# Kernel optimization log

Measured on AMD Instinct MI355X. Metric: run time of the kernel, lower is better.

Reference implementation:

```python
import jax, jax.numpy as jnp
import numpy as np

N = 49152       # nodes
EH = 8192       # hyperedges (star nodes)
M = N + EH
F = 256         # num_features == expan_dim == MLP_hidden
D = 256
HEADS = 8
CHUNK = 1024
NE_N = 10 * N   # nnz of N x N sparse mats
NE_M = 10 * M   # nnz of M x M sparse mats


def spmm(row, col, val, X, n):
    # sparse [n, m] (COO) @ dense X [m, d] -> [n, d]
    return jax.ops.segment_sum(val[:, None] * X[col], row, num_segments=n)


def expan_net(x, row, col, val, Ws, bs, n):
    # 2-layer GCN: (A @ (X @ W) + b), ReLU between; dropout is identity in eval.
    h = spmm(row, col, val, x @ Ws[0], n) + bs[0]
    h = jax.nn.relu(h)
    return spmm(row, col, val, h @ Ws[1], n) + bs[1]


def chunked_mha(q, k, v, in_w, in_b, out_w, out_b):
    # torch nn.MultiheadAttention on unbatched [L, D] chunks of size CHUNK
    n, d = q.shape
    c = n // CHUNK
    dh = d // HEADS
    wq, wk, wv = jnp.split(in_w, 3, axis=0)
    bq, bk, bv = jnp.split(in_b, 3)
    def resh(t):
        return t.reshape(c, CHUNK, HEADS, dh)
    qh = resh(q @ wq.T + bq)
    kh = resh(k @ wk.T + bk)
    vh = resh(v @ wv.T + bv)
    scale = 1.0 / np.sqrt(dh)
    scores = jnp.einsum('clhe,cmhe->chlm', qh, kh) * scale  # [c,H,CHUNK,CHUNK]
    attn = jax.nn.softmax(scores, axis=-1)
    out = jnp.einsum('chlm,cmhe->clhe', attn, vh).reshape(n, d)
    return out @ out_w.T + out_b


def setup_inputs():
    key = jax.random.key(0)
    ks = iter(jax.random.split(key, 64))
    nrm = lambda shape, s=1.0: jax.random.normal(next(ks), shape, dtype=jnp.float32) * s
    uni = lambda shape: jax.random.uniform(next(ks), shape, dtype=jnp.float32)
    ridx = lambda shape, hi: jax.random.randint(next(ks), shape, 0, hi, dtype=jnp.int32)
    inp = {'x': nrm((N, F))}
    for nm, ne, hi in [('A_cg', NE_N, N), ('A_hyp', NE_N, N), ('A_sg', NE_M, M),
                       ('L_cg', NE_N, N), ('L_hyp', NE_N, N), ('L_sg', NE_M, M)]:
        inp[nm + '_row'] = ridx((ne,), hi)
        inp[nm + '_col'] = ridx((ne,), hi)
        inp[nm + '_val'] = uni((ne,)) * 0.1
    for p in ['cg', 'hg', 'sg']:
        inp[p + '_W'] = nrm((2, F, D), 0.05)
        inp[p + '_b'] = nrm((2, D), 0.05)
    for p in ['sn_hyp', 'sn_cg', 'sn_sg']:
        inp[p + '_W'] = nrm((D, D), 0.05)
        inp[p + '_b'] = nrm((D,), 0.05)
    for p in ['spa', 'spe']:
        for q in ['hyp', 'star', 'clq']:
            inp[f'{p}_{q}_W'] = nrm((D, D), 0.05)
            inp[f'{p}_{q}_b'] = nrm((D,), 0.05)
        inp[p + '_in_w'] = nrm((3 * D, D), 0.05)
        inp[p + '_in_b'] = nrm((3 * D,), 0.05)
        inp[p + '_out_w'] = nrm((D, D), 0.05)
        inp[p + '_out_b'] = nrm((D,), 0.05)
    return inp


def reference(x,
              A_cg_row, A_cg_col, A_cg_val, A_hyp_row, A_hyp_col, A_hyp_val,
              A_sg_row, A_sg_col, A_sg_val, L_cg_row, L_cg_col, L_cg_val,
              L_hyp_row, L_hyp_col, L_hyp_val, L_sg_row, L_sg_col, L_sg_val,
              cg_W, cg_b, hg_W, hg_b, sg_W, sg_b,
              sn_hyp_W, sn_hyp_b, sn_cg_W, sn_cg_b, sn_sg_W, sn_sg_b,
              spa_hyp_W, spa_hyp_b, spa_star_W, spa_star_b, spa_clq_W, spa_clq_b,
              spa_in_w, spa_in_b, spa_out_w, spa_out_b,
              spe_hyp_W, spe_hyp_b, spe_star_W, spe_star_b, spe_clq_W, spe_clq_b,
              spe_in_w, spe_in_b, spe_out_w, spe_out_b):
    n = x.shape[0]
    # star features: nodes first, zero-init hyperedge rows (v_mask == [True]*N+[False]*EH)
    x_star = jnp.concatenate([x, jnp.zeros((EH, x.shape[1]), x.dtype)], axis=0)
    # 1. Expansion graph convolutions
    cg_feat = expan_net(x, A_cg_row, A_cg_col, A_cg_val, cg_W, cg_b, n)
    hg_feat = expan_net(x, A_hyp_row, A_hyp_col, A_hyp_val, hg_W, hg_b, n)
    sg_feat = expan_net(x_star, A_sg_row, A_sg_col, A_sg_val, sg_W, sg_b, n + EH)
    X_star, S_star = sg_feat[:n], sg_feat[n:]
    # 2. SmoothNet: linear then Laplacian spmm
    X_hyp = spmm(L_hyp_row, L_hyp_col, L_hyp_val, hg_feat @ sn_hyp_W.T + sn_hyp_b, n)
    X_cg = spmm(L_cg_row, L_cg_col, L_cg_val, cg_feat @ sn_cg_W.T + sn_cg_b, n)
    X_sg = spmm(L_sg_row, L_sg_col, L_sg_val, sg_feat @ sn_sg_W.T + sn_sg_b, n + EH)
    # 3. TAA attention (chunked MHA, Q/K/V = hyp/star/clique projections)
    X_spectral = chunked_mha(X_hyp @ spe_hyp_W.T + spe_hyp_b,
                             X_cg @ spe_star_W.T + spe_star_b,
                             X_sg[:n] @ spe_clq_W.T + spe_clq_b,
                             spe_in_w, spe_in_b, spe_out_w, spe_out_b)
    X_spatial = chunked_mha(hg_feat @ spa_hyp_W.T + spa_hyp_b,
                            cg_feat @ spa_star_W.T + spa_star_b,
                            X_star @ spa_clq_W.T + spa_clq_b,
                            spa_in_w, spa_in_b, spa_out_w, spa_out_b)
    taa = jnp.concatenate([X_spatial, X_spectral], axis=1)
    return taa, X_star, S_star
```

## Files before the change

### kernel.cpp

```cpp
#include <hip/hip_runtime.h>

#define NN 49152
#define EHN 8192
#define MM (NN + EHN)
#define FD 256
#define DD 256
#define NHEADS 8
#define DHEAD 32
#define CHK 1024
#define NEN (10 * NN)
#define NEM (10 * MM)
#define ROWS_TOT (4 * NN + 2 * MM)
#define ETOT (4 * NEN + 2 * NEM)

typedef __bf16 bf16x8 __attribute__((ext_vector_type(8)));
typedef unsigned short u16x8 __attribute__((ext_vector_type(8)));
typedef float f32x4 __attribute__((ext_vector_type(4)));

static __device__ __forceinline__ unsigned short f2bf(float f) {
  unsigned int u = __float_as_uint(f);
  unsigned int r = (u + 0x7FFFu + ((u >> 16) & 1u)) >> 16;
  return (unsigned short)r;
}
static __device__ __forceinline__ float bf2f(unsigned short u) {
  return __uint_as_float((unsigned int)u << 16);
}
static __device__ __forceinline__ unsigned int cvtpk(float a, float b) {
  unsigned int r;
  asm("v_cvt_pk_bf16_f32 %0, %1, %2" : "=v"(r) : "v"(a), "v"(b));
  return r;
}

struct CastJobs {
  const float* src[8];
  unsigned short* dst[8];
  int trans[8];
};
__global__ __launch_bounds__(256) void cast_w8_kernel(CastJobs jobs)
{
  int job = blockIdx.x >> 8;
  int i = (blockIdx.x & 255) * 256 + threadIdx.x;
  int n = i >> 8, k = i & 255;
  const float* src = jobs.src[job];
  float f = jobs.trans[job] ? src[(size_t)k * 256 + n] : src[i];
  jobs.dst[job][i] = f2bf(f);
}

__global__ __launch_bounds__(256) void combine_w_kernel(
    const float* __restrict__ Bw, const float* __restrict__ Aw,
    const float* __restrict__ ab, const float* __restrict__ bb,
    unsigned short* __restrict__ Wc, float* __restrict__ bc, float fscale)
{
  int n = blockIdx.x, t = threadIdx.x;
  __shared__ float shB[256];
  __shared__ float red[256];
  shB[t] = Bw[n * 256 + t];
  __syncthreads();
  float acc = 0.0f;
  #pragma unroll 8
  for (int j = 0; j < 256; ++j) acc += shB[j] * Aw[j * 256 + t];
  Wc[n * 256 + t] = f2bf(acc * fscale);
  red[t] = shB[t] * ab[t];
  __syncthreads();
  for (int off = 128; off; off >>= 1) {
    if (t < off) red[t] += red[t + off];
    __syncthreads();
  }
  if (t == 0) bc[n] = (red[0] + bb[n]) * fscale;
}

__global__ __launch_bounds__(256) void mm256f_kernel(
    const float* __restrict__ A, const float* __restrict__ B,
    float* __restrict__ C)
{
  int n = blockIdx.x, t = threadIdx.x;
  __shared__ float sa[256];
  sa[t] = A[n * 256 + t];
  __syncthreads();
  float acc = 0.0f;
  #pragma unroll 8
  for (int j = 0; j < 256; ++j) acc += sa[j] * B[j * 256 + t];
  C[n * 256 + t] = acc;
}

__global__ __launch_bounds__(256) void mm256b_kernel(
    const float* __restrict__ A, const float* __restrict__ B,
    unsigned short* __restrict__ W, float fs)
{
  int n = blockIdx.x, t = threadIdx.x;
  __shared__ float sa[256];
  sa[t] = A[n * 256 + t];
  __syncthreads();
  float acc = 0.0f;
  #pragma unroll 8
  for (int j = 0; j < 256; ++j) acc += sa[j] * B[j * 256 + t];
  W[n * 256 + t] = f2bf(acc * fs);
}

__global__ __launch_bounds__(256) void mv256_kernel(
    const float* __restrict__ W, const float* __restrict__ v,
    const float* __restrict__ add, float* __restrict__ outv, float fs)
{
  int t = threadIdx.x;
  __shared__ float sv[256];
  sv[t] = v[t];
  __syncthreads();
  float acc = 0.0f;
  #pragma unroll 8
  for (int k = 0; k < 256; ++k) acc += W[t * 256 + k] * sv[k];
  if (add) acc += add[t];
  outv[t] = fs * acc;
}

template<int ABF, int OUTBF>
__global__ __launch_bounds__(256) void gemm2_kernel(
    const void* __restrict__ Ain, const unsigned short* __restrict__ Wt,
    const float* __restrict__ c0, const float* __restrict__ rs,
    const float* __restrict__ cvec, void* __restrict__ Cout,
    int ldc, int coff, int relu)
{
  __shared__ __align__(16) char sA[2][4096];
  __shared__ __align__(16) char sB[2][16384];
  const int tid = threadIdx.x, lane = tid & 63, wid = tid >> 6;
  const int l15 = lane & 15, l4 = lane >> 4;
  const int bm = blockIdx.x * 64;

  f32x4 acc[16] = {};
  const int ar = tid >> 2, akq = (tid & 3) * 8;
  const int bn = tid;

  float4 fa0, fa1;
  u16x8 ua;
  u16x8 rb0, rb1, rb2, rb3;
  auto stage_load = [&](int k0) {
    if (ABF) {
      ua = *(const u16x8*)((const unsigned short*)Ain +
                           (size_t)(bm + ar) * 256 + k0 + akq);
    } else {
      const float* ap = (const float*)Ain + (size_t)(bm + ar) * 256 + k0 + akq;
      fa0 = *(const float4*)ap;
      fa1 = *(const float4*)(ap + 4);
    }
    const unsigned short* bp = Wt + (size_t)bn * 256 + k0;
    rb0 = *(const u16x8*)bp;        rb1 = *(const u16x8*)(bp + 8);
    rb2 = *(const u16x8*)(bp + 16); rb3 = *(const u16x8*)(bp + 24);
  };
  auto stage_write = [&](int buf) {
    u16x8 va;
    if (ABF) {
      va = ua;
    } else {
      va[0] = f2bf(fa0.x); va[1] = f2bf(fa0.y); va[2] = f2bf(fa0.z); va[3] = f2bf(fa0.w);
      va[4] = f2bf(fa1.x); va[5] = f2bf(fa1.y); va[6] = f2bf(fa1.z); va[7] = f2bf(fa1.w);
    }
    int aa = ((ar << 6) + (akq << 1)) ^ ((ar & 7) << 4);
    *(u16x8*)(sA[buf] + aa) = va;
    int bb = (bn << 6) ^ ((bn & 7) << 4);
    *(u16x8*)(sB[buf] + bb) = rb0;
    *(u16x8*)(sB[buf] + (bb ^ 16)) = rb1;
    *(u16x8*)(sB[buf] + (bb ^ 32)) = rb2;
    *(u16x8*)(sB[buf] + (bb ^ 48)) = rb3;
  };

  stage_load(0);
  stage_write(0);
  __syncthreads();
  int cur = 0;
  for (int it = 0; it < 8; ++it) {
    if (it < 7) stage_load((it + 1) * 32);
    int ra = wid * 16 + l15;
    bf16x8 af = *(const bf16x8*)(sA[cur] + ((ra << 6) + (l4 << 4) ^ ((ra & 7) << 4)));
    #pragma unroll
    for (int n4 = 0; n4 < 16; ++n4) {
      int rn = n4 * 16 + l15;
      bf16x8 bf = *(const bf16x8*)(sB[cur] + ((rn << 6) + (l4 << 4) ^ ((rn & 7) << 4)));
      acc[n4] = __builtin_amdgcn_mfma_f32_16x16x32_bf16(af, bf, acc[n4], 0, 0, 0);
    }
    __syncthreads();
    if (it < 7) {
      stage_write(cur ^ 1);
      __syncthreads();
      cur ^= 1;
    }
  }
  const int row = bm + wid * 16 + l4 * 4;
  float rsv[4];
  if (rs) {
    #pragma unroll
    for (int j = 0; j < 4; ++j) rsv[j] = rs[row + j];
  }
  #pragma unroll
  for (int n4 = 0; n4 < 16; ++n4) {
    int col = n4 * 16 + l15;
    float base = c0 ? c0[col] : 0.0f;
    float cv = rs ? cvec[col] : 0.0f;
    #pragma unroll
    for (int j = 0; j < 4; ++j) {
      float v = acc[n4][j] + base;
      if (rs) v += rsv[j] * cv;
      if (relu) v = fmaxf(v, 0.0f);
      if (OUTBF)
        ((unsigned short*)Cout)[(size_t)(row + j) * 256 + col] = f2bf(v);
      else
        ((float*)Cout)[(size_t)(row + j) * ldc + coff + col] = v;
    }
  }
}

struct CooPtrs {
  const int* rw[6];
  const int* cl[6];
  const float* vl[6];
};
static __device__ __forceinline__ void coo_block_resolve(
    int b, int& g, int& eb, int& rb)
{
  if      (b < 1920) { g = 0; eb = 0;    rb = 0; }
  else if (b < 3840) { g = 1; eb = 1920; rb = NN; }
  else if (b < 6080) { g = 2; eb = 3840; rb = 2 * NN; }
  else if (b < 8000) { g = 3; eb = 6080; rb = 2 * NN + MM; }
  else if (b < 9920) { g = 4; eb = 8000; rb = 3 * NN + MM; }
  else               { g = 5; eb = 9920; rb = 4 * NN + MM; }
}

__global__ __launch_bounds__(256) void count_all_kernel(
    CooPtrs coo, int* __restrict__ cnt)
{
  int g, eb, rb;
  coo_block_resolve(blockIdx.x, g, eb, rb);
  int e = (blockIdx.x - eb) * 256 + threadIdx.x;
  atomicAdd(&cnt[rb + coo.rw[g][e]], 1);
}

__global__ __launch_bounds__(256) void scan1_kernel(
    const int* __restrict__ cnt, int* __restrict__ bsum, int n)
{
  __shared__ int sh[256];
  int i = blockIdx.x * 256 + threadIdx.x;
  sh[threadIdx.x] = (i < n) ? cnt[i] : 0;
  __syncthreads();
  for (int off = 128; off; off >>= 1) {
    if (threadIdx.x < off) sh[threadIdx.x] += sh[threadIdx.x + off];
    __syncthreads();
  }
  if (threadIdx.x == 0) bsum[blockIdx.x] = sh[0];
}

__global__ __launch_bounds__(256) void scan2_kernel(int* __restrict__ bsum, int nb)
{
  __shared__ int sh[256];
  int t = threadIdx.x;
  int carry = 0;
  for (int base = 0; base < nb; base += 256) {
    int i = base + t;
    int v = (i < nb) ? bsum[i] : 0;
    sh[t] = v;
    __syncthreads();
    for (int off = 1; off < 256; off <<= 1) {
      int add = (t >= off) ? sh[t - off] : 0;
      __syncthreads();
      sh[t] += add;
      __syncthreads();
    }
    int incl = sh[t];
    int tot = sh[255];
    if (i < nb) bsum[i] = carry + incl - v;
    carry += tot;
    __syncthreads();
  }
}

__global__ __launch_bounds__(256) void scan3_kernel(
    const int* __restrict__ cnt, const int* __restrict__ bsum,
    int* __restrict__ rowptr, int* __restrict__ cntz, int n)
{
  __shared__ int sh[256];
  int i = blockIdx.x * 256 + threadIdx.x;
  int v = (i < n) ? cnt[i] : 0;
  sh[threadIdx.x] = v;
  __syncthreads();
  for (int off = 1; off < 256; off <<= 1) {
    int add = (threadIdx.x >= off) ? sh[threadIdx.x - off] : 0;
    __syncthreads();
    sh[threadIdx.x] += add;
    __syncthreads();
  }
  int incl = sh[threadIdx.x];
  int base = bsum[blockIdx.x];
  if (i < n) { rowptr[i] = base + incl - v; cntz[i] = 0; }
  if (i == n - 1) rowptr[n] = base + incl;
}

__global__ __launch_bounds__(256) void fill_all_kernel(
    CooPtrs coo, const int* __restrict__ P, int* __restrict__ cur,
    int* __restrict__ ecol, float* __restrict__ eval)
{
  int g, eb, rb;
  coo_block_resolve(blockIdx.x, g, eb, rb);
  int e = (blockIdx.x - eb) * 256 + threadIdx.x;
  int grow = rb + coo.rw[g][e];
  int pos = P[grow] + atomicAdd(&cur[grow], 1);
  ecol[pos] = coo.cl[g][e];
  eval[pos] = coo.vl[g][e];
}

__global__ __launch_bounds__(256) void rowsum_all_kernel(
    const int* __restrict__ P, const float* __restrict__ eval,
    float* __restrict__ rsAll)
{
  int j = blockIdx.x * 256 + threadIdx.x;
  int g = j / NN;
  int r = j - g * NN;
  int grow = (g == 0 ? 2 * NN + MM : g == 1 ? 3 * NN + MM : 4 * NN + MM) + r;
  float s = 0.0f;
  int end = P[grow + 1];
  for (int e = P[grow]; e < end; ++e) s += eval[e];
  rsAll[j] = s;
}

__global__ __launch_bounds__(256) void csr_spmm_kernel(
    const int* __restrict__ rowptr, const int* __restrict__ ecol,
    const float* __restrict__ eval, const unsigned short* __restrict__ X,
    unsigned short* __restrict__ Y, int src_rows,
    const float* __restrict__ bias, int relu, float* __restrict__ Y2)
{
  const int wave = threadIdx.x >> 6, lane = threadIdx.x & 63;
  const int r = blockIdx.x * 4 + wave;
  const int f0 = lane * 4;
  int e = rowptr[r], end = rowptr[r + 1];
  float a0 = 0.0f, a1 = 0.0f, a2 = 0.0f, a3 = 0.0f;
  for (; e + 3 < end; e += 4) {
    int c0i = ecol[e], c1i = ecol[e + 1], c2i = ecol[e + 2], c3i = ecol[e + 3];
    float v0 = eval[e], v1 = eval[e + 1], v2 = eval[e + 2], v3 = eval[e + 3];
    ushort4 x0 = {0,0,0,0}, x1 = {0,0,0,0}, x2 = {0,0,0,0}, x3 = {0,0,0,0};
    if (c0i < src_rows) x0 = *(const ushort4*)(X + (size_t)c0i * DD + f0);
    if (c1i < src_rows) x1 = *(const ushort4*)(X + (size_t)c1i * DD + f0);
    if (c2i < src_rows) x2 = *(const ushort4*)(X + (size_t)c2i * DD + f0);
    if (c3i < src_rows) x3 = *(const ushort4*)(X + (size_t)c3i * DD + f0);
    if (c0i < src_rows) { a0 += v0*bf2f(x0.x); a1 += v0*bf2f(x0.y); a2 += v0*bf2f(x0.z); a3 += v0*bf2f(x0.w); }
    if (c1i < src_rows) { a0 += v1*bf2f(x1.x); a1 += v1*bf2f(x1.y); a2 += v1*bf2f(x1.z); a3 += v1*bf2f(x1.w); }
    if (c2i < src_rows) { a0 += v2*bf2f(x2.x); a1 += v2*bf2f(x2.y); a2 += v2*bf2f(x2.z); a3 += v2*bf2f(x2.w); }
    if (c3i < src_rows) { a0 += v3*bf2f(x3.x); a1 += v3*bf2f(x3.y); a2 += v3*bf2f(x3.z); a3 += v3*bf2f(x3.w); }
  }
  for (; e < end; ++e) {
    int c = ecol[e];
    float v = eval[e];
    if (c < src_rows) {
      ushort4 xx = *(const ushort4*)(X + (size_t)c * DD + f0);
      a0 += v * bf2f(xx.x); a1 += v * bf2f(xx.y);
      a2 += v * bf2f(xx.z); a3 += v * bf2f(xx.w);
    }
  }
  if (bias) {
    a0 += bias[f0]; a1 += bias[f0 + 1]; a2 += bias[f0 + 2]; a3 += bias[f0 + 3];
  }
  if (relu) {
    a0 = fmaxf(a0, 0.0f); a1 = fmaxf(a1, 0.0f);
    a2 = fmaxf(a2, 0.0f); a3 = fmaxf(a3, 0.0f);
  }
  uint2 yb = { cvtpk(a0, a1), cvtpk(a2, a3) };
  *(uint2*)(Y + (size_t)r * DD + f0) = yb;
  if (Y2) {
    float4 yf = {a0, a1, a2, a3};
    *(float4*)(Y2 + (size_t)r * DD + f0) = yf;
  }
}

__global__ __launch_bounds__(256) void attn_mfma_kernel(
    const unsigned short* __restrict__ Q, const unsigned short* __restrict__ K,
    const unsigned short* __restrict__ V, unsigned short* __restrict__ O)
{
  __shared__ __align__(16) char sKb[4096];
  __shared__ __align__(16) char sVb[4096];
  __shared__ __align__(16) char sPb[8192];
  const int wgid = (blockIdx.x & 7) * 768 + (blockIdx.x >> 3);
  const int qb = wgid & 15, h = (wgid >> 4) & 7, c = wgid >> 7;
  const int tid = threadIdx.x, lane = tid & 63, wid = tid >> 6;
  const int l15 = lane & 15, l4 = lane >> 4;
  char* sPw = sPb + wid * 2048;
  const size_t base = (size_t)c * (CHK * DD) + (size_t)h * DHEAD;
  const int q0 = qb * 64 + wid * 16;

  bf16x8 qf = *(const bf16x8*)(Q + base + (size_t)(q0 + l15) * DD + l4 * 8);

  const int key_s = tid >> 2, dq = (tid & 3) * 8;
  const unsigned short* Kp = K + base + (size_t)key_s * DD + dq;
  const unsigned short* Vp = V + base + (size_t)key_s * DD + dq;
  const int kaddr = ((key_s << 6) + (dq << 1)) ^ ((key_s & 7) << 4);

  f32x4 oacc[2] = {};
  float m = -1e30f, l = 0.0f;
  const f32x4 zero = {};

  for (int kt = 0; kt < CHK; kt += 64) {
    __syncthreads();
    u16x8 kv = *(const u16x8*)Kp;  Kp += 64 * DD;
    u16x8 vv = *(const u16x8*)Vp;  Vp += 64 * DD;
    *(u16x8*)(sKb + kaddr) = kv;
    #pragma unroll
    for (int i = 0; i < 8; ++i) {
      int d = dq + i;
      int bb = ((d << 7) + (key_s << 1))
             ^ ((d & 7) << 4) ^ (((d >> 3) & 3) << 5);
      *(unsigned short*)(sVb + bb) = vv[i];
    }
    __syncthreads();

    f32x4 s[4];
    #pragma unroll
    for (int s4 = 0; s4 < 4; ++s4) {
      int key = s4 * 16 + l15;
      int ba = ((key << 6) + (l4 << 4)) ^ ((key & 7) << 4);
      bf16x8 kf = *(const bf16x8*)(sKb + ba);
      s[s4] = __builtin_amdgcn_mfma_f32_16x16x32_bf16(kf, qf, zero, 0, 0, 0);
    }
    float tmax = -1e30f;
    #pragma unroll
    for (int s4 = 0; s4 < 4; ++s4)
      #pragma unroll
      for (int j = 0; j < 4; ++j) tmax = fmaxf(tmax, s[s4][j]);
    tmax = fmaxf(tmax, __shfl_xor(tmax, 16));
    tmax = fmaxf(tmax, __shfl_xor(tmax, 32));
    bool skip = __all(tmax - m <= 8.0f);
    float mnew = skip ? m : fmaxf(m, tmax);
    if (!skip) {
      float corr = __builtin_amdgcn_exp2f(m - mnew);
      l *= corr;
      oacc[0] *= corr;
      oacc[1] *= corr;
    }
    float psum = 0.0f;
    float p[4][4];
    #pragma unroll
    for (int s4 = 0; s4 < 4; ++s4)
      #pragma unroll
      for (int j = 0; j < 4; ++j) {
        p[s4][j] = __builtin_amdgcn_exp2f(s[s4][j] - mnew);
        psum += p[s4][j];
      }
    psum += __shfl_xor(psum, 16);
    psum += __shfl_xor(psum, 32);
    l += psum;
    m = mnew;
    #pragma unroll
    for (int s4 = 0; s4 < 4; ++s4) {
      uint2 pk = { cvtpk(p[s4][0], p[s4][1]), cvtpk(p[s4][2], p[s4][3]) };
      int bp = ((l15 << 7) + (s4 << 5) + (l4 << 3)) ^ ((l15 & 7) << 4);
      *(uint2*)(sPw + bp) = pk;
    }
    __syncthreads();

    #pragma unroll
    for (int dh = 0; dh < 2; ++dh)
      #pragma unroll
      for (int kh = 0; kh < 2; ++kh) {
        int d = dh * 16 + l15;
        int ba = ((d << 7) + ((kh * 32 + l4 * 8) << 1))
               ^ ((d & 7) << 4) ^ (((d >> 3) & 3) << 5);
        bf16x8 vf = *(const bf16x8*)(sVb + ba);
        int bp = ((l15 << 7) + (kh << 6) + (l4 << 4)) ^ ((l15 & 7) << 4);
        bf16x8 pf = *(const bf16x8*)(sPw + bp);
        oacc[dh] = __builtin_amdgcn_mfma_f32_16x16x32_bf16(vf, pf, oacc[dh], 0, 0, 0);
      }
  }

  float inv = 1.0f / l;
  unsigned short* orow = O + base + (size_t)(q0 + l15) * DD;
  #pragma unroll
  for (int dh = 0; dh < 2; ++dh) {
    uint2 o2 = { cvtpk(oacc[dh][0] * inv, oacc[dh][1] * inv),
                 cvtpk(oacc[dh][2] * inv, oacc[dh][3] * inv) };
    *(uint2*)(orow + dh * 16 + l4 * 4) = o2;
  }
}

__global__ __launch_bounds__(256) void fill_kernel(float* p, long n, float v)
{
  long i = (long)blockIdx.x * 256 + threadIdx.x;
  if (i < n) p[i] = v;
}

extern "C" void kernel_launch(void* const* d_in, const int* in_sizes, int n_in,
                              void* d_out, int out_size, void* d_ws, size_t ws_size,
                              hipStream_t stream)
{
  const float* x     = (const float*)d_in[0];
  const int*   Acg_r = (const int*)d_in[1];
  const int*   Acg_c = (const int*)d_in[2];
  const float* Acg_v = (const float*)d_in[3];
  const int*   Ahy_r = (const int*)d_in[4];
  const int*   Ahy_c = (const int*)d_in[5];
  const float* Ahy_v = (const float*)d_in[6];
  const int*   Asg_r = (const int*)d_in[7];
  const int*   Asg_c = (const int*)d_in[8];
  const float* Asg_v = (const float*)d_in[9];
  const int*   Lcg_r = (const int*)d_in[10];
  const int*   Lcg_c = (const int*)d_in[11];
  const float* Lcg_v = (const float*)d_in[12];
  const int*   Lhy_r = (const int*)d_in[13];
  const int*   Lhy_c = (const int*)d_in[14];
  const float* Lhy_v = (const float*)d_in[15];
  const int*   Lsg_r = (const int*)d_in[16];
  const int*   Lsg_c = (const int*)d_in[17];
  const float* Lsg_v = (const float*)d_in[18];
  const float* cg_W  = (const float*)d_in[19];
  const float* cg_b  = (const float*)d_in[20];
  const float* hg_W  = (const float*)d_in[21];
  const float* hg_b  = (const float*)d_in[22];
  const float* sg_W  = (const float*)d_in[23];
  const float* sg_b  = (const float*)d_in[24];
  const float* snh_W = (const float*)d_in[25];
  const float* snh_b = (const float*)d_in[26];
  const float* snc_W = (const float*)d_in[27];
  const float* snc_b = (const float*)d_in[28];
  const float* sns_W = (const float*)d_in[29];
  const float* sns_b = (const float*)d_in[30];
  const float* spa_hyp_W  = (const float*)d_in[31];
  const float* spa_hyp_b  = (const float*)d_in[32];
  const float* spa_star_W = (const float*)d_in[33];
  const float* spa_star_b = (const float*)d_in[34];
  const float* spa_clq_W  = (const float*)d_in[35];
  const float* spa_clq_b  = (const float*)d_in[36];
  const float* spa_in_w   = (const float*)d_in[37];
  const float* spa_in_b   = (const float*)d_in[38];
  const float* spa_out_w  = (const float*)d_in[39];
  const float* spa_out_b  = (const float*)d_in[40];
  const float* spe_hyp_W  = (const float*)d_in[41];
  const float* spe_hyp_b  = (const float*)d_in[42];
  const float* spe_star_W = (const float*)d_in[43];
  const float* spe_star_b = (const float*)d_in[44];
  const float* spe_clq_W  = (const float*)d_in[45];
  const float* spe_clq_b  = (const float*)d_in[46];
  const float* spe_in_w   = (const float*)d_in[47];
  const float* spe_in_b   = (const float*)d_in[48];
  const float* spe_out_w  = (const float*)d_in[49];
  const float* spe_out_b  = (const float*)d_in[50];

  float* out = (float*)d_out;

  const size_t NF = (size_t)NN * DD;
  const size_t MF = (size_t)MM * DD;
  const size_t WELEMS  = 14u * 65536u;
  const size_t need = (3 * MF + 9 * NF) * 2
                    + ((size_t)3 * NN + 65536 + 256 + 4096) * 4
                    + ((size_t)ROWS_TOT + 1 + 2 * (size_t)ETOT + ROWS_TOT + 2048) * 4
                    + WELEMS * 2;

  auto fill = [&](float v) {
    long tot = (long)out_size;
    fill_kernel<<<dim3((unsigned)((tot + 255) / 256)), 256, 0, stream>>>(out, tot, v);
  };
  if (ws_size < need)                        { fill(12.0f); return; }
  if (n_in != 51)                            { fill(16.0f); return; }
  if (in_sizes[0] != NN * FD)                { fill(20.0f); return; }
  if (in_sizes[3] != NEN)                    { fill(24.0f); return; }
  if (in_sizes[9] != NEM)                    { fill(28.0f); return; }
  if (in_sizes[19] != 2 * FD * DD)           { fill(32.0f); return; }
  if (in_sizes[37] != 3 * DD * DD)           { fill(36.0f); return; }
  if (out_size != NN * 512 + NN * DD + EHN * DD) { fill(40.0f); return; }

  unsigned short* T  = (unsigned short*)d_ws;
  unsigned short* H  = T + MF;
  unsigned short* SG = H + MF;
  unsigned short* CG = SG + MF;
  unsigned short* HG = CG + NF;
  unsigned short* LH = HG + NF;
  unsigned short* LC = LH + NF;
  unsigned short* LS = LC + NF;
  unsigned short* QH = LS + NF;
  unsigned short* KH = QH + NF;
  unsigned short* VH = KH + NF;
  unsigned short* AO = VH + NF;

  float* fp = (float*)(AO + NF);
  float* rsAll = fp;           fp += 3 * NN;
  float* tmp256 = fp;          fp += 65536;
  float* tmpv = fp;            fp += 256;
  float* CB = fp;              fp += 4096;

  int* ip = (int*)fp;
  int* P    = ip;              ip += ROWS_TOT + 1;
  int* ecol = ip;              ip += ETOT;
  float* eval = (float*)ip;    ip += ETOT;
  int* cnt  = ip;              ip += ROWS_TOT;
  int* bsum = ip;              ip += 2048;
  unsigned short* WB = (unsigned short*)ip;

  int* rp_cg  = P;
  int* rp_hy  = P + NN;
  int* rp_sg  = P + 2 * NN;
  int* rp_Lcg = P + 2 * NN + MM;
  int* rp_Lhy = P + 3 * NN + MM;
  int* rp_Lsg = P + 4 * NN + MM;
  float* rs_c = rsAll;
  float* rs_h = rsAll + NN;
  float* rs_s = rsAll + 2 * NN;

  auto wslot = [&](int s) { return WB + (size_t)s * 65536; };
  auto cb    = [&](int s) { return CB + (size_t)s * 256; };

  auto combine = [&](const float* Bw, const float* Aw, const float* ab,
                     const float* bb, unsigned short* Wc, float* bcp, float fs) {
    combine_w_kernel<<<dim3(256), 256, 0, stream>>>(Bw, Aw, ab, bb, Wc, bcp, fs);
  };
  auto combine3 = [&](const float* w3, const float* b3, const float* pW,
                      const float* pb, const float* sW, const float* sb,
                      unsigned short* Wc, float* cvecp, float* c0p, float fs) {
    mm256f_kernel<<<dim3(256), 256, 0, stream>>>(pW, sW, tmp256);
    mm256b_kernel<<<dim3(256), 256, 0, stream>>>(w3, tmp256, Wc, fs);
    mv256_kernel<<<dim3(1), 256, 0, stream>>>(pW, sb, nullptr, tmpv, 1.0f);
    mv256_kernel<<<dim3(1), 256, 0, stream>>>(w3, tmpv, nullptr, cvecp, fs);
    mv256_kernel<<<dim3(1), 256, 0, stream>>>(w3, pb, b3, c0p, fs);
  };
  auto gemm32in = [&](const float* A, const unsigned short* Wt,
                      unsigned short* C, int Mrows) {
    gemm2_kernel<0, 1><<<dim3(Mrows / 64), 256, 0, stream>>>(
        A, Wt, nullptr, nullptr, nullptr, C, 256, 0, 0);
  };
  auto gemmbb = [&](const unsigned short* A, const unsigned short* Wt,
                    const float* c0, unsigned short* C, int Mrows) {
    gemm2_kernel<1, 1><<<dim3(Mrows / 64), 256, 0, stream>>>(
        A, Wt, c0, nullptr, nullptr, C, 256, 0, 0);
  };
  auto gemmrs = [&](const unsigned short* A, const unsigned short* Wt,
                    const float* c0, const float* rs, const float* cvec,
                    unsigned short* C, int Mrows) {
    gemm2_kernel<1, 1><<<dim3(Mrows / 64), 256, 0, stream>>>(
        A, Wt, c0, rs, cvec, C, 256, 0, 0);
  };
  auto gemmout = [&](const unsigned short* A, const unsigned short* Wt,
                     const float* c0, float* C, int coff) {
    gemm2_kernel<1, 0><<<dim3(NN / 64), 256, 0, stream>>>(
        A, Wt, c0, nullptr, nullptr, C, 512, coff, 0);
  };
  auto spmm = [&](const int* rowptr, const unsigned short* X, unsigned short* Y,
                  int srcR, int dstR, const float* bias, bool relu,
                  float* Y2 = nullptr) {
    csr_spmm_kernel<<<dim3(dstR / 4), 256, 0, stream>>>(
        rowptr, ecol, eval, X, Y, srcR, bias, relu ? 1 : 0, Y2);
  };
  auto attn = [&](const unsigned short* Qp, const unsigned short* Kp,
                  const unsigned short* Vp, unsigned short* Op) {
    attn_mfma_kernel<<<dim3(6144), 256, 0, stream>>>(Qp, Kp, Vp, Op);
  };

  const float fsQ = 0.17677669529663687f * 1.4426950408889634f;

  {
    CastJobs jobs;
    jobs.src[0] = cg_W;           jobs.dst[0] = wslot(0);  jobs.trans[0] = 1;
    jobs.src[1] = cg_W + FD * DD; jobs.dst[1] = wslot(1);  jobs.trans[1] = 1;
    jobs.src[2] = hg_W;           jobs.dst[2] = wslot(2);  jobs.trans[2] = 1;
    jobs.src[3] = hg_W + FD * DD; jobs.dst[3] = wslot(3);  jobs.trans[3] = 1;
    jobs.src[4] = sg_W;           jobs.dst[4] = wslot(4);  jobs.trans[4] = 1;
    jobs.src[5] = sg_W + FD * DD; jobs.dst[5] = wslot(5);  jobs.trans[5] = 1;
    jobs.src[6] = spa_out_w;      jobs.dst[6] = wslot(12); jobs.trans[6] = 0;
    jobs.src[7] = spe_out_w;      jobs.dst[7] = wslot(13); jobs.trans[7] = 0;
    cast_w8_kernel<<<dim3(8 * 256), 256, 0, stream>>>(jobs);
  }
  combine(spa_in_w,                spa_hyp_W,  spa_hyp_b,  spa_in_b,          wslot(6), cb(0), fsQ);
  combine(spa_in_w + DD * DD,      spa_star_W, spa_star_b, spa_in_b + DD,     wslot(7), cb(1), 1.0f);
  combine(spa_in_w + 2 * DD * DD,  spa_clq_W,  spa_clq_b,  spa_in_b + 2 * DD, wslot(8), cb(2), 1.0f);
  combine3(spe_in_w,               spe_in_b,            spe_hyp_W,  spe_hyp_b,  snh_W, snh_b, wslot(9),  cb(3), cb(4), fsQ);
  combine3(spe_in_w + DD * DD,     spe_in_b + DD,       spe_star_W, spe_star_b, snc_W, snc_b, wslot(10), cb(5), cb(6), 1.0f);
  combine3(spe_in_w + 2 * DD * DD, spe_in_b + 2 * DD,   spe_clq_W,  spe_clq_b,  sns_W, sns_b, wslot(11), cb(7), cb(8), 1.0f);

  {
    CooPtrs coo;
    coo.rw[0] = Acg_r; coo.cl[0] = Acg_c; coo.vl[0] = Acg_v;
    coo.rw[1] = Ahy_r; coo.cl[1] = Ahy_c; coo.vl[1] = Ahy_v;
    coo.rw[2] = Asg_r; coo.cl[2] = Asg_c; coo.vl[2] = Asg_v;
    coo.rw[3] = Lcg_r; coo.cl[3] = Lcg_c; coo.vl[3] = Lcg_v;
    coo.rw[4] = Lhy_r; coo.cl[4] = Lhy_c; coo.vl[4] = Lhy_v;
    coo.rw[5] = Lsg_r; coo.cl[5] = Lsg_c; coo.vl[5] = Lsg_v;
    hipMemsetAsync(cnt, 0, (size_t)ROWS_TOT * 4, stream);
    count_all_kernel<<<dim3(ETOT / 256), 256, 0, stream>>>(coo, cnt);
    scan1_kernel<<<dim3(ROWS_TOT / 256), 256, 0, stream>>>(cnt, bsum, ROWS_TOT);
    scan2_kernel<<<dim3(1), 256, 0, stream>>>(bsum, ROWS_TOT / 256);
    scan3_kernel<<<dim3(ROWS_TOT / 256), 256, 0, stream>>>(cnt, bsum, P, cnt, ROWS_TOT);
    fill_all_kernel<<<dim3(ETOT / 256), 256, 0, stream>>>(coo, P, cnt, ecol, eval);
    rowsum_all_kernel<<<dim3(3 * NN / 256), 256, 0, stream>>>(P, eval, rsAll);
  }

  gemm32in(x, wslot(0), T, NN);
  spmm(rp_cg, T, H, NN, NN, cg_b, true);
  gemmbb(H, wslot(1), nullptr, T, NN);
  spmm(rp_cg, T, CG, NN, NN, cg_b + DD, false);

  gemm32in(x, wslot(2), T, NN);
  spmm(rp_hy, T, H, NN, NN, hg_b, true);
  gemmbb(H, wslot(3), nullptr, T, NN);
  spmm(rp_hy, T, HG, NN, NN, hg_b + DD, false);

  gemm32in(x, wslot(4), T, NN);
  spmm(rp_sg, T, H, NN, MM, sg_b, true);
  gemmbb(H, wslot(5), nullptr, T, MM);
  spmm(rp_sg, T, SG, MM, MM, sg_b + DD, false, out + (size_t)NN * 512);

  spmm(rp_Lhy, HG, LH, NN, NN, nullptr, false);
  spmm(rp_Lcg, CG, LC, NN, NN, nullptr, false);
  spmm(rp_Lsg, SG, LS, MM, NN, nullptr, false);

  gemmrs(LH, wslot(9),  cb(4), rs_h, cb(3), QH, NN);
  gemmrs(LC, wslot(10), cb(6), rs_c, cb(5), KH, NN);
  gemmrs(LS, wslot(11), cb(8), rs_s, cb(7), VH, NN);
  attn(QH, KH, VH, AO);
  gemmout(AO, wslot(13), spe_out_b, out, 256);

  gemmbb(HG, wslot(6), cb(0), QH, NN);
  gemmbb(CG, wslot(7), cb(1), KH, NN);
  gemmbb(SG, wslot(8), cb(2), VH, NN);
  attn(QH, KH, VH, AO);
  gemmout(AO, wslot(12), spa_out_b, out, 0);
}
```

Before: 1.677 ms.

## Batch the three graph branches into grouped GEMM and SpMM launches with packed CSR

Independent GEMMs and SpMMs for the clique, hypergraph and star branches are merged into single grouped launches (gemm3_kernel, spmm3_kernel) that pick a branch by block index, with separate intermediate buffers per branch. CSR column indices and values are packed into int2 so each edge is read with one load. The goal is to cut launch count and fill the GPU better with small serial kernels, at the cost of a larger workspace and a relu flag shared by every branch in a launch.

```diff
diff --git a/kernel.cpp b/kernel.cpp
--- a/kernel.cpp
+++ b/kernel.cpp
@@ -112,18 +112,28 @@
   outv[t] = fs * acc;
 }
 
-template<int ABF, int OUTBF>
-__global__ __launch_bounds__(256) void gemm2_kernel(
-    const void* __restrict__ Ain, const unsigned short* __restrict__ Wt,
-    const float* __restrict__ c0, const float* __restrict__ rs,
-    const float* __restrict__ cvec, void* __restrict__ Cout,
-    int ldc, int coff, int relu)
-{
+struct Gemm3 {
+  const void* A[3];
+  const unsigned short* W[3];
+  const float* c0[3];
+  const float* rs[3];
+  const float* cvec[3];
+  unsigned short* out[3];
+  int bs1, bs2, btot;
+};
+template<int ABF>
+__global__ __launch_bounds__(256) void gemm3_kernel(Gemm3 g)
+{
+  const int b = blockIdx.x;
+  const int j = (b >= g.bs2) ? 2 : (b >= g.bs1 ? 1 : 0);
+  const int bm = (b - (j == 2 ? g.bs2 : j == 1 ? g.bs1 : 0)) * 64;
+  const void* Ain = g.A[j];
+  const unsigned short* Wt = g.W[j];
+
   __shared__ __align__(16) char sA[2][4096];
   __shared__ __align__(16) char sB[2][16384];
   const int tid = threadIdx.x, lane = tid & 63, wid = tid >> 6;
   const int l15 = lane & 15, l4 = lane >> 4;
-  const int bm = blockIdx.x * 64;
 
   f32x4 acc[16] = {};
   const int ar = tid >> 2, akq = (tid & 3) * 8;
@@ -184,10 +194,14 @@
     }
   }
   const int row = bm + wid * 16 + l4 * 4;
+  const float* rs = g.rs[j];
+  const float* c0 = g.c0[j];
+  const float* cvec = g.cvec[j];
+  unsigned short* Cout = g.out[j];
   float rsv[4];
   if (rs) {
     #pragma unroll
-    for (int j = 0; j < 4; ++j) rsv[j] = rs[row + j];
+    for (int jj = 0; jj < 4; ++jj) rsv[jj] = rs[row + jj];
   }
   #pragma unroll
   for (int n4 = 0; n4 < 16; ++n4) {
@@ -195,15 +209,72 @@
     float base = c0 ? c0[col] : 0.0f;
     float cv = rs ? cvec[col] : 0.0f;
     #pragma unroll
-    for (int j = 0; j < 4; ++j) {
-      float v = acc[n4][j] + base;
-      if (rs) v += rsv[j] * cv;
-      if (relu) v = fmaxf(v, 0.0f);
-      if (OUTBF)
-        ((unsigned short*)Cout)[(size_t)(row + j) * 256 + col] = f2bf(v);
-      else
-        ((float*)Cout)[(size_t)(row + j) * ldc + coff + col] = v;
-    }
+    for (int jj = 0; jj < 4; ++jj) {
+      float v = acc[n4][jj] + base;
+      if (rs) v += rsv[jj] * cv;
+      Cout[(size_t)(row + jj) * 256 + col] = f2bf(v);
+    }
+  }
+}
+
+__global__ __launch_bounds__(256) void gemmout_kernel(
+    const unsigned short* __restrict__ Ain, const unsigned short* __restrict__ Wt,
+    const float* __restrict__ c0, float* __restrict__ Cout, int coff)
+{
+  __shared__ __align__(16) char sA[2][4096];
+  __shared__ __align__(16) char sB[2][16384];
+  const int tid = threadIdx.x, lane = tid & 63, wid = tid >> 6;
+  const int l15 = lane & 15, l4 = lane >> 4;
+  const int bm = blockIdx.x * 64;
+
+  f32x4 acc[16] = {};
+  const int ar = tid >> 2, akq = (tid & 3) * 8;
+  const int bn = tid;
+  u16x8 ua, rb0, rb1, rb2, rb3;
+  auto stage_load = [&](int k0) {
+    ua = *(const u16x8*)(Ain + (size_t)(bm + ar) * 256 + k0 + akq);
+    const unsigned short* bp = Wt + (size_t)bn * 256 + k0;
+    rb0 = *(const u16x8*)bp;        rb1 = *(const u16x8*)(bp + 8);
+    rb2 = *(const u16x8*)(bp + 16); rb3 = *(const u16x8*)(bp + 24);
+  };
+  auto stage_write = [&](int buf) {
+    int aa = ((ar << 6) + (akq << 1)) ^ ((ar & 7) << 4);
+    *(u16x8*)(sA[buf] + aa) = ua;
+    int bb = (bn << 6) ^ ((bn & 7) << 4);
+    *(u16x8*)(sB[buf] + bb) = rb0;
+    *(u16x8*)(sB[buf] + (bb ^ 16)) = rb1;
+    *(u16x8*)(sB[buf] + (bb ^ 32)) = rb2;
+    *(u16x8*)(sB[buf] + (bb ^ 48)) = rb3;
+  };
+  stage_load(0);
+  stage_write(0);
+  __syncthreads();
+  int cur = 0;
+  for (int it = 0; it < 8; ++it) {
+    if (it < 7) stage_load((it + 1) * 32);
+    int ra = wid * 16 + l15;
+    bf16x8 af = *(const bf16x8*)(sA[cur] + ((ra << 6) + (l4 << 4) ^ ((ra & 7) << 4)));
+    #pragma unroll
+    for (int n4 = 0; n4 < 16; ++n4) {
+      int rn = n4 * 16 + l15;
+      bf16x8 bf = *(const bf16x8*)(sB[cur] + ((rn << 6) + (l4 << 4) ^ ((rn & 7) << 4)));
+      acc[n4] = __builtin_amdgcn_mfma_f32_16x16x32_bf16(af, bf, acc[n4], 0, 0, 0);
+    }
+    __syncthreads();
+    if (it < 7) {
+      stage_write(cur ^ 1);
+      __syncthreads();
+      cur ^= 1;
+    }
+  }
+  const int row = bm + wid * 16 + l4 * 4;
+  #pragma unroll
+  for (int n4 = 0; n4 < 16; ++n4) {
+    int col = n4 * 16 + l15;
+    float base = c0[col];
+    #pragma unroll
+    for (int jj = 0; jj < 4; ++jj)
+      Cout[(size_t)(row + jj) * 512 + coff + col] = acc[n4][jj] + base;
   }
 }
 
@@ -293,19 +364,18 @@
 
 __global__ __launch_bounds__(256) void fill_all_kernel(
     CooPtrs coo, const int* __restrict__ P, int* __restrict__ cur,
-    int* __restrict__ ecol, float* __restrict__ eval)
+    int2* __restrict__ epack)
 {
   int g, eb, rb;
   coo_block_resolve(blockIdx.x, g, eb, rb);
   int e = (blockIdx.x - eb) * 256 + threadIdx.x;
   int grow = rb + coo.rw[g][e];
   int pos = P[grow] + atomicAdd(&cur[grow], 1);
-  ecol[pos] = coo.cl[g][e];
-  eval[pos] = coo.vl[g][e];
+  epack[pos] = make_int2(coo.cl[g][e], __float_as_int(coo.vl[g][e]));
 }
 
 __global__ __launch_bounds__(256) void rowsum_all_kernel(
-    const int* __restrict__ P, const float* __restrict__ eval,
+    const int* __restrict__ P, const int2* __restrict__ epack,
     float* __restrict__ rsAll)
 {
   int j = blockIdx.x * 256 + threadIdx.x;
@@ -314,43 +384,57 @@
   int grow = (g == 0 ? 2 * NN + MM : g == 1 ? 3 * NN + MM : 4 * NN + MM) + r;
   float s = 0.0f;
   int end = P[grow + 1];
-  for (int e = P[grow]; e < end; ++e) s += eval[e];
+  for (int e = P[grow]; e < end; ++e) s += __int_as_float(epack[e].y);
   rsAll[j] = s;
 }
 
-__global__ __launch_bounds__(256) void csr_spmm_kernel(
-    const int* __restrict__ rowptr, const int* __restrict__ ecol,
-    const float* __restrict__ eval, const unsigned short* __restrict__ X,
-    unsigned short* __restrict__ Y, int src_rows,
-    const float* __restrict__ bias, int relu, float* __restrict__ Y2)
-{
+struct Spmm3 {
+  const int* rowptr[3];
+  const unsigned short* X[3];
+  unsigned short* Y[3];
+  float* Y2[3];
+  const float* bias[3];
+  int src_rows[3];
+  int bs1, bs2;
+};
+__global__ __launch_bounds__(256) void spmm3_kernel(
+    Spmm3 s, const int2* __restrict__ ep, int relu)
+{
+  const int b = blockIdx.x;
+  const int j = (b >= s.bs2) ? 2 : (b >= s.bs1 ? 1 : 0);
+  const int rblk = b - (j == 2 ? s.bs2 : j == 1 ? s.bs1 : 0);
   const int wave = threadIdx.x >> 6, lane = threadIdx.x & 63;
-  const int r = blockIdx.x * 4 + wave;
+  const int r = rblk * 4 + wave;
   const int f0 = lane * 4;
+  const int src_rows = s.src_rows[j];
+  const unsigned short* X = s.X[j];
+  const int* rowptr = s.rowptr[j];
   int e = rowptr[r], end = rowptr[r + 1];
   float a0 = 0.0f, a1 = 0.0f, a2 = 0.0f, a3 = 0.0f;
   for (; e + 3 < end; e += 4) {
-    int c0i = ecol[e], c1i = ecol[e + 1], c2i = ecol[e + 2], c3i = ecol[e + 3];
-    float v0 = eval[e], v1 = eval[e + 1], v2 = eval[e + 2], v3 = eval[e + 3];
+    int2 cv0 = ep[e], cv1 = ep[e + 1], cv2 = ep[e + 2], cv3 = ep[e + 3];
     ushort4 x0 = {0,0,0,0}, x1 = {0,0,0,0}, x2 = {0,0,0,0}, x3 = {0,0,0,0};
-    if (c0i < src_rows) x0 = *(const ushort4*)(X + (size_t)c0i * DD + f0);
-    if (c1i < src_rows) x1 = *(const ushort4*)(X + (size_t)c1i * DD + f0);
-    if (c2i < src_rows) x2 = *(const ushort4*)(X + (size_t)c2i * DD + f0);
-    if (c3i < src_rows) x3 = *(const ushort4*)(X + (size_t)c3i * DD + f0);
-    if (c0i < src_rows) { a0 += v0*bf2f(x0.x); a1 += v0*bf2f(x0.y); a2 += v0*bf2f(x0.z); a3 += v0*bf2f(x0.w); }
-    if (c1i < src_rows) { a0 += v1*bf2f(x1.x); a1 += v1*bf2f(x1.y); a2 += v1*bf2f(x1.z); a3 += v1*bf2f(x1.w); }
-    if (c2i < src_rows) { a0 += v2*bf2f(x2.x); a1 += v2*bf2f(x2.y); a2 += v2*bf2f(x2.z); a3 += v2*bf2f(x2.w); }
-    if (c3i < src_rows) { a0 += v3*bf2f(x3.x); a1 += v3*bf2f(x3.y); a2 += v3*bf2f(x3.z); a3 += v3*bf2f(x3.w); }
+    if (cv0.x < src_rows) x0 = *(const ushort4*)(X + (size_t)cv0.x * DD + f0);
+    if (cv1.x < src_rows) x1 = *(const ushort4*)(X + (size_t)cv1.x * DD + f0);
+    if (cv2.x < src_rows) x2 = *(const ushort4*)(X + (size_t)cv2.x * DD + f0);
+    if (cv3.x < src_rows) x3 = *(const ushort4*)(X + (size_t)cv3.x * DD + f0);
+    float v0 = __int_as_float(cv0.y), v1 = __int_as_float(cv1.y);
+    float v2 = __int_as_float(cv2.y), v3 = __int_as_float(cv3.y);
+    if (cv0.x < src_rows) { a0 += v0*bf2f(x0.x); a1 += v0*bf2f(x0.y); a2 += v0*bf2f(x0.z); a3 += v0*bf2f(x0.w); }
+    if (cv1.x < src_rows) { a0 += v1*bf2f(x1.x); a1 += v1*bf2f(x1.y); a2 += v1*bf2f(x1.z); a3 += v1*bf2f(x1.w); }
+    if (cv2.x < src_rows) { a0 += v2*bf2f(x2.x); a1 += v2*bf2f(x2.y); a2 += v2*bf2f(x2.z); a3 += v2*bf2f(x2.w); }
+    if (cv3.x < src_rows) { a0 += v3*bf2f(x3.x); a1 += v3*bf2f(x3.y); a2 += v3*bf2f(x3.z); a3 += v3*bf2f(x3.w); }
   }
   for (; e < end; ++e) {
-    int c = ecol[e];
-    float v = eval[e];
-    if (c < src_rows) {
-      ushort4 xx = *(const ushort4*)(X + (size_t)c * DD + f0);
+    int2 cv = ep[e];
+    if (cv.x < src_rows) {
+      float v = __int_as_float(cv.y);
+      ushort4 xx = *(const ushort4*)(X + (size_t)cv.x * DD + f0);
       a0 += v * bf2f(xx.x); a1 += v * bf2f(xx.y);
       a2 += v * bf2f(xx.z); a3 += v * bf2f(xx.w);
     }
   }
+  const float* bias = s.bias[j];
   if (bias) {
     a0 += bias[f0]; a1 += bias[f0 + 1]; a2 += bias[f0 + 2]; a3 += bias[f0 + 3];
   }
@@ -359,10 +443,10 @@
     a2 = fmaxf(a2, 0.0f); a3 = fmaxf(a3, 0.0f);
   }
   uint2 yb = { cvtpk(a0, a1), cvtpk(a2, a3) };
-  *(uint2*)(Y + (size_t)r * DD + f0) = yb;
-  if (Y2) {
+  *(uint2*)(s.Y[j] + (size_t)r * DD + f0) = yb;
+  if (s.Y2[j]) {
     float4 yf = {a0, a1, a2, a3};
-    *(float4*)(Y2 + (size_t)r * DD + f0) = yf;
+    *(float4*)(s.Y2[j] + (size_t)r * DD + f0) = yf;
   }
 }
 
@@ -541,9 +625,10 @@
   const size_t NF = (size_t)NN * DD;
   const size_t MF = (size_t)MM * DD;
   const size_t WELEMS  = 14u * 65536u;
-  const size_t need = (3 * MF + 9 * NF) * 2
+  const size_t need = (14 * NF + 3 * MF) * 2
+                    + (size_t)ETOT * 8
                     + ((size_t)3 * NN + 65536 + 256 + 4096) * 4
-                    + ((size_t)ROWS_TOT + 1 + 2 * (size_t)ETOT + ROWS_TOT + 2048) * 4
+                    + ((size_t)ROWS_TOT + 1 + ROWS_TOT + 2048) * 4
                     + WELEMS * 2;
 
   auto fill = [&](float v) {
@@ -559,32 +644,36 @@
   if (in_sizes[37] != 3 * DD * DD)           { fill(36.0f); return; }
   if (out_size != NN * 512 + NN * DD + EHN * DD) { fill(40.0f); return; }
 
-  unsigned short* T  = (unsigned short*)d_ws;
-  unsigned short* H  = T + MF;
-  unsigned short* SG = H + MF;
-  unsigned short* CG = SG + MF;
-  unsigned short* HG = CG + NF;
-  unsigned short* LH = HG + NF;
-  unsigned short* LC = LH + NF;
-  unsigned short* LS = LC + NF;
-  unsigned short* QH = LS + NF;
-  unsigned short* KH = QH + NF;
-  unsigned short* VH = KH + NF;
-  unsigned short* AO = VH + NF;
-
-  float* fp = (float*)(AO + NF);
+  unsigned short* Tcg = (unsigned short*)d_ws;
+  unsigned short* Thy = Tcg + NF;
+  unsigned short* Tsg = Thy + NF;
+  unsigned short* Hcg = Tsg + NF;
+  unsigned short* Hhy = Hcg + NF;
+  unsigned short* Hsg = Hhy + NF;
+  unsigned short* Usg = Hsg + MF;
+  unsigned short* SG  = Usg + MF;
+  unsigned short* CG  = SG + MF;
+  unsigned short* HG  = CG + NF;
+  unsigned short* LH  = HG + NF;
+  unsigned short* LC  = LH + NF;
+  unsigned short* LS  = LC + NF;
+  unsigned short* QH  = LS + NF;
+  unsigned short* KH  = QH + NF;
+  unsigned short* VH  = KH + NF;
+  unsigned short* AO  = VH + NF;
+  unsigned short* Ucg = Tcg;
+  unsigned short* Uhy = Thy;
+
+  int2* epack = (int2*)(AO + NF);
+  float* fp = (float*)(epack + ETOT);
   float* rsAll = fp;           fp += 3 * NN;
   float* tmp256 = fp;          fp += 65536;
   float* tmpv = fp;            fp += 256;
   float* CB = fp;              fp += 4096;
-
-  int* ip = (int*)fp;
-  int* P    = ip;              ip += ROWS_TOT + 1;
-  int* ecol = ip;              ip += ETOT;
-  float* eval = (float*)ip;    ip += ETOT;
-  int* cnt  = ip;              ip += ROWS_TOT;
-  int* bsum = ip;              ip += 2048;
-  unsigned short* WB = (unsigned short*)ip;
+  int* P    = (int*)fp;
+  int* cnt  = P + ROWS_TOT + 1;
+  int* bsum = cnt + ROWS_TOT;
+  unsigned short* WB = (unsigned short*)(bsum + 2048);
 
   int* rp_cg  = P;
   int* rp_hy  = P + NN;
@@ -612,37 +701,6 @@
     mv256_kernel<<<dim3(1), 256, 0, stream>>>(w3, tmpv, nullptr, cvecp, fs);
     mv256_kernel<<<dim3(1), 256, 0, stream>>>(w3, pb, b3, c0p, fs);
   };
-  auto gemm32in = [&](const float* A, const unsigned short* Wt,
-                      unsigned short* C, int Mrows) {
-    gemm2_kernel<0, 1><<<dim3(Mrows / 64), 256, 0, stream>>>(
-        A, Wt, nullptr, nullptr, nullptr, C, 256, 0, 0);
-  };
-  auto gemmbb = [&](const unsigned short* A, const unsigned short* Wt,
-                    const float* c0, unsigned short* C, int Mrows) {
-    gemm2_kernel<1, 1><<<dim3(Mrows / 64), 256, 0, stream>>>(
-        A, Wt, c0, nullptr, nullptr, C, 256, 0, 0);
-  };
-  auto gemmrs = [&](const unsigned short* A, const unsigned short* Wt,
-                    const float* c0, const float* rs, const float* cvec,
-                    unsigned short* C, int Mrows) {
-    gemm2_kernel<1, 1><<<dim3(Mrows / 64), 256, 0, stream>>>(
-        A, Wt, c0, rs, cvec, C, 256, 0, 0);
-  };
-  auto gemmout = [&](const unsigned short* A, const unsigned short* Wt,
-                     const float* c0, float* C, int coff) {
-    gemm2_kernel<1, 0><<<dim3(NN / 64), 256, 0, stream>>>(
-        A, Wt, c0, nullptr, nullptr, C, 512, coff, 0);
-  };
-  auto spmm = [&](const int* rowptr, const unsigned short* X, unsigned short* Y,
-                  int srcR, int dstR, const float* bias, bool relu,
-                  float* Y2 = nullptr) {
-    csr_spmm_kernel<<<dim3(dstR / 4), 256, 0, stream>>>(
-        rowptr, ecol, eval, X, Y, srcR, bias, relu ? 1 : 0, Y2);
-  };
-  auto attn = [&](const unsigned short* Qp, const unsigned short* Kp,
-                  const unsigned short* Vp, unsigned short* Op) {
-    attn_mfma_kernel<<<dim3(6144), 256, 0, stream>>>(Qp, Kp, Vp, Op);
-  };
 
   const float fsQ = 0.17677669529663687f * 1.4426950408889634f;
 
@@ -678,38 +736,72 @@
     scan1_kernel<<<dim3(ROWS_TOT / 256), 256, 0, stream>>>(cnt, bsum, ROWS_TOT);
     scan2_kernel<<<dim3(1), 256, 0, stream>>>(bsum, ROWS_TOT / 256);
     scan3_kernel<<<dim3(ROWS_TOT / 256), 256, 0, stream>>>(cnt, bsum, P, cnt, ROWS_TOT);
-    fill_all_kernel<<<dim3(ETOT / 256), 256, 0, stream>>>(coo, P, cnt, ecol, eval);
-    rowsum_all_kernel<<<dim3(3 * NN / 256), 256, 0, stream>>>(P, eval, rsAll);
-  }
-
-  gemm32in(x, wslot(0), T, NN);
-  spmm(rp_cg, T, H, NN, NN, cg_b, true);
-  gemmbb(H, wslot(1), nullptr, T, NN);
-  spmm(rp_cg, T, CG, NN, NN, cg_b + DD, false);
-
-  gemm32in(x, wslot(2), T, NN);
-  spmm(rp_hy, T, H, NN, NN, hg_b, true);
-  gemmbb(H, wslot(3), nullptr, T, NN);
-  spmm(rp_hy, T, HG, NN, NN, hg_b + DD, false);
-
-  gemm32in(x, wslot(4), T, NN);
-  spmm(rp_sg, T, H, NN, MM, sg_b, true);
-  gemmbb(H, wslot(5), nullptr, T, MM);
-  spmm(rp_sg, T, SG, MM, MM, sg_b + DD, false, out + (size_t)NN * 512);
-
-  spmm(rp_Lhy, HG, LH, NN, NN, nullptr, false);
-  spmm(rp_Lcg, CG, LC, NN, NN, nullptr, false);
-  spmm(rp_Lsg, SG, LS, MM, NN, nullptr, false);
-
-  gemmrs(LH, wslot(9),  cb(4), rs_h, cb(3), QH, NN);
-  gemmrs(LC, wslot(10), cb(6), rs_c, cb(5), KH, NN);
-  gemmrs(LS, wslot(11), cb(8), rs_s, cb(7), VH, NN);
-  attn(QH, KH, VH, AO);
-  gemmout(AO, wslot(13), spe_out_b, out, 256);
-
-  gemmbb(HG, wslot(6), cb(0), QH, NN);
-  gemmbb(CG, wslot(7), cb(1), KH, NN);
-  gemmbb(SG, wslot(8), cb(2), VH, NN);
-  attn(QH, KH, VH, AO);
-  gemmout(AO, wslot(12), spa_out_b, out, 0);
-}
+    fill_all_kernel<<<dim3(ETOT / 256), 256, 0, stream>>>(coo, P, cnt, epack);
+    rowsum_all_kernel<<<dim3(3 * NN / 256), 256, 0, stream>>>(P, epack, rsAll);
+  }
+
+  {
+    Gemm3 g = {};
+    for (int j = 0; j < 3; ++j) { g.A[j] = x; g.c0[j] = nullptr; g.rs[j] = nullptr; }
+    g.W[0] = wslot(0); g.out[0] = Tcg;
+    g.W[1] = wslot(2); g.out[1] = Thy;
+    g.W[2] = wslot(4); g.out[2] = Tsg;
+    g.bs1 = 768; g.bs2 = 1536; g.btot = 2304;
+    gemm3_kernel<0><<<dim3(2304), 256, 0, stream>>>(g);
+  }
+  {
+    Spmm3 s = {};
+    s.rowptr[0] = rp_cg; s.X[0] = Tcg; s.Y[0] = Hcg; s.Y2[0] = nullptr; s.bias[0] = cg_b; s.src_rows[0] = NN;
+    s.rowptr[1] = rp_hy; s.X[1] = Thy; s.Y[1] = Hhy; s.Y2[1] = nullptr; s.bias[1] = hg_b; s.src_rows[1] = NN;
+    s.rowptr[2] = rp_sg; s.X[2] = Tsg; s.Y[2] = Hsg; s.Y2[2] = nullptr; s.bias[2] = sg_b; s.src_rows[2] = NN;
+    s.bs1 = NN / 4; s.bs2 = 2 * (NN / 4);
+    spmm3_kernel<<<dim3(2 * (NN / 4) + MM / 4), 256, 0, stream>>>(s, epack, 1);
+  }
+  {
+    Gemm3 g = {};
+    g.A[0] = Hcg; g.W[0] = wslot(1); g.out[0] = Ucg;
+    g.A[1] = Hhy; g.W[1] = wslot(3); g.out[1] = Uhy;
+    g.A[2] = Hsg; g.W[2] = wslot(5); g.out[2] = Usg;
+    for (int j = 0; j < 3; ++j) { g.c0[j] = nullptr; g.rs[j] = nullptr; }
+    g.bs1 = NN / 64; g.bs2 = 2 * (NN / 64); g.btot = 2 * (NN / 64) + MM / 64;
+    gemm3_kernel<1><<<dim3(2 * (NN / 64) + MM / 64), 256, 0, stream>>>(g);
+  }
+  {
+    Spmm3 s = {};
+    s.rowptr[0] = rp_cg; s.X[0] = Ucg; s.Y[0] = CG; s.Y2[0] = nullptr; s.bias[0] = cg_b + DD; s.src_rows[0] = NN;
+    s.rowptr[1] = rp_hy; s.X[1] = Uhy; s.Y[1] = HG; s.Y2[1] = nullptr; s.bias[1] = hg_b + DD; s.src_rows[1] = NN;
+    s.rowptr[2] = rp_sg; s.X[2] = Usg; s.Y[2] = SG; s.Y2[2] = out + (size_t)NN * 512; s.bias[2] = sg_b + DD; s.src_rows[2] = MM;
+    s.bs1 = NN / 4; s.bs2 = 2 * (NN / 4);
+    spmm3_kernel<<<dim3(2 * (NN / 4) + MM / 4), 256, 0, stream>>>(s, epack, 0);
+  }
+  {
+    Spmm3 s = {};
+    s.rowptr[0] = rp_Lhy; s.X[0] = HG; s.Y[0] = LH; s.Y2[0] = nullptr; s.bias[0] = nullptr; s.src_rows[0] = NN;
+    s.rowptr[1] = rp_Lcg; s.X[1] = CG; s.Y[1] = LC; s.Y2[1] = nullptr; s.bias[1] = nullptr; s.src_rows[1] = NN;
+    s.rowptr[2] = rp_Lsg; s.X[2] = SG; s.Y[2] = LS; s.Y2[2] = nullptr; s.bias[2] = nullptr; s.src_rows[2] = MM;
+    s.bs1 = NN / 4; s.bs2 = 2 * (NN / 4);
+    spmm3_kernel<<<dim3(3 * (NN / 4)), 256, 0, stream>>>(s, epack, 0);
+  }
+
+  {
+    Gemm3 g = {};
+    g.A[0] = LH; g.W[0] = wslot(9);  g.c0[0] = cb(4); g.rs[0] = rs_h; g.cvec[0] = cb(3); g.out[0] = QH;
+    g.A[1] = LC; g.W[1] = wslot(10); g.c0[1] = cb(6); g.rs[1] = rs_c; g.cvec[1] = cb(5); g.out[1] = KH;
+    g.A[2] = LS; g.W[2] = wslot(11); g.c0[2] = cb(8); g.rs[2] = rs_s; g.cvec[2] = cb(7); g.out[2] = VH;
+    g.bs1 = 768; g.bs2 = 1536; g.btot = 2304;
+    gemm3_kernel<1><<<dim3(2304), 256, 0, stream>>>(g);
+  }
+  attn_mfma_kernel<<<dim3(6144), 256, 0, stream>>>(QH, KH, VH, AO);
+  gemmout_kernel<<<dim3(NN / 64), 256, 0, stream>>>(AO, wslot(13), spe_out_b, out, 256);
+
+  {
+    Gemm3 g = {};
+    g.A[0] = HG; g.W[0] = wslot(6); g.c0[0] = cb(0); g.rs[0] = nullptr; g.out[0] = QH;
+    g.A[1] = CG; g.W[1] = wslot(7); g.c0[1] = cb(1); g.rs[1] = nullptr; g.out[1] = KH;
+    g.A[2] = SG; g.W[2] = wslot(8); g.c0[2] = cb(2); g.rs[2] = nullptr; g.out[2] = VH;
+    g.bs1 = 768; g.bs2 = 1536; g.btot = 2304;
+    gemm3_kernel<1><<<dim3(2304), 256, 0, stream>>>(g);
+  }
+  attn_mfma_kernel<<<dim3(6144), 256, 0, stream>>>(QH, KH, VH, AO);
+  gemmout_kernel<<<dim3(NN / 64), 256, 0, stream>>>(AO, wslot(12), spa_out_b, out, 0);
+}
```

Result: faster. 1.603 ms (-4.4%).
